# Kernel tuning notes

Hardware: AMD Instinct MI355X
Metric: run time of the kernel (lower is better)

Reference implementation:

```python
import jax, jax.numpy as jnp
import numpy as np
from functools import partial

# Straight-through sign (Binarize): sign forward, identity gradient
@jax.custom_vjp
def ste_sign(x):
    return jnp.sign(x)

def _ste_fwd(x):
    return jnp.sign(x), None

def _ste_bwd(_, g):
    return (g,)

ste_sign.defvjp(_ste_fwd, _ste_bwd)


def conv2d(x, w):
    # x: [N,C,H,W], w: [O,I,kh,kw], VALID conv, stride 1
    return jax.lax.conv_general_dilated(
        x, w, window_strides=(1, 1), padding='VALID',
        dimension_numbers=('NCHW', 'OIHW', 'NCHW'))


def maxpool2x2(x):
    return jax.lax.reduce_window(
        x, -jnp.inf, jax.lax.max, (1, 1, 2, 2), (1, 1, 2, 2), 'VALID')


def setup_inputs() -> dict:
    key = jax.random.key(0)
    ks = jax.random.split(key, 32)
    d = {}
    d['x'] = jax.random.normal(ks[0], (128, 3, 32, 32), dtype=jnp.float32)
    wshapes = [(128, 3, 3, 3), (128, 128, 3, 3), (256, 128, 3, 3),
               (256, 256, 3, 3), (512, 256, 3, 3), (512, 512, 3, 3),
               (10, 512, 4, 4)]
    for i, s in enumerate(wshapes):
        d[f'w{i+1}'] = jax.random.normal(ks[1 + i], s, dtype=jnp.float32) * 0.05
    bn_ch = [128, 128, 256, 256, 512, 512, 10]
    for i, c in enumerate(bn_ch):
        d[f'bn{i+1}_s'] = jax.random.uniform(ks[10 + 2 * i], (c,), dtype=jnp.float32,
                                             minval=0.5, maxval=1.5)
        d[f'bn{i+1}_t'] = jax.random.normal(ks[11 + 2 * i], (c,), dtype=jnp.float32) * 0.1
    return d


def _forward(x, w1, w2, w3, w4, w5, w6, w7,
             bn1_s, bn1_t, bn2_s, bn2_t, bn3_s, bn3_t, bn4_s, bn4_t,
             bn5_s, bn5_t, bn6_s, bn6_t, bn7_s, bn7_t):
    def block(h, w, s, t, pool, binarize_in):
        if binarize_in:
            h = ste_sign(h)            # binarize activations (in_ch != 3)
        h = jnp.pad(h, ((0, 0), (0, 0), (1, 1), (1, 1)))  # F.pad value=0
        h = conv2d(h, ste_sign(w))      # binarized weights
        if pool:
            h = maxpool2x2(h)
        h = h * s[None, :, None, None] + t[None, :, None, None]  # eval BN
        return jnp.clip(h, -1.0, 1.0)   # Hardtanh

    h = block(x, w1, bn1_s, bn1_t, pool=False, binarize_in=False)  # 32x32x128
    h = block(h, w2, bn2_s, bn2_t, pool=True,  binarize_in=True)   # 16x16x128
    h = block(h, w3, bn3_s, bn3_t, pool=False, binarize_in=True)   # 16x16x256
    h = block(h, w4, bn4_s, bn4_t, pool=True,  binarize_in=True)   # 8x8x256
    h = block(h, w5, bn5_s, bn5_t, pool=False, binarize_in=True)   # 8x8x512
    h = block(h, w6, bn6_s, bn6_t, pool=True,  binarize_in=True)   # 4x4x512
    # conv7: binarize input + weights, 4x4 kernel, no padding -> [N,10,1,1]
    h = conv2d(ste_sign(h), ste_sign(w7))
    h = h.reshape(-1, 10)
    h = h * bn7_s + bn7_t               # eval BatchNorm1d(10)
    return jax.nn.log_softmax(h, axis=1)


def reference(x, w1, w2, w3, w4, w5, w6, w7,
              bn1_s, bn1_t, bn2_s, bn2_t, bn3_s, bn3_t, bn4_s, bn4_t,
              bn5_s, bn5_t, bn6_s, bn6_t, bn7_s, bn7_t):
    return _forward(x, w1, w2, w3, w4, w5, w6, w7,
                    bn1_s, bn1_t, bn2_s, bn2_t, bn3_s, bn3_t, bn4_s, bn4_t,
                    bn5_s, bn5_t, bn6_s, bn6_t, bn7_s, bn7_t)
```

## Files before the change

kernel.cpp:

```cpp
#include <hip/hip_runtime.h>
#include <cstdint>
#include <math.h>

#define NB 128

__global__ void pack_all_kernel(
    const float* __restrict__ w2, const float* __restrict__ w3,
    const float* __restrict__ w4, const float* __restrict__ w5,
    const float* __restrict__ w6, const float* __restrict__ w7,
    uint32_t* __restrict__ wp2, uint32_t* __restrict__ wp3,
    uint32_t* __restrict__ wp4, uint32_t* __restrict__ wp5,
    uint32_t* __restrict__ wp6, uint32_t* __restrict__ wp7) {
  int i = blockIdx.x * 256 + threadIdx.x;
  const float* w; uint32_t* wp; int C, KHW; bool nl = true;
  if (i < 4608)        { w = w2; wp = wp2; C = 128; KHW = 9; }
  else if (i < 13824)  { i -= 4608;   w = w3; wp = wp3; C = 128; KHW = 9; }
  else if (i < 32256)  { i -= 13824;  w = w4; wp = wp4; C = 256; KHW = 9; }
  else if (i < 69120)  { i -= 32256;  w = w5; wp = wp5; C = 256; KHW = 9; }
  else if (i < 142848) { i -= 69120;  w = w6; wp = wp6; C = 512; KHW = 9; }
  else if (i < 145408) { i -= 142848; w = w7; wp = wp7; C = 512; KHW = 16; nl = false; }
  else return;
  int Cw = C >> 5;
  int cw = i % Cw;
  int rest = i / Cw;
  int t = rest % KHW;
  int o = rest / KHW;
  uint32_t word = 0;
  for (int b = 0; b < 32; ++b)
    word |= ((w[(o * C + cw * 32 + b) * KHW + t] >= 0.0f) ? 1u : 0u) << b;
  if (nl) wp[(((o >> 6) * KHW + t) * Cw + cw) * 64 + (o & 63)] = word;
  else    wp[(o * KHW + t) * Cw + cw] = word;
}

__global__ __launch_bounds__(256) void conv1_kernel(
    const float* __restrict__ x, const float* __restrict__ w1,
    const float* __restrict__ bs, const float* __restrict__ bt,
    uint32_t* __restrict__ out) {
  const int ocw = blockIdx.y;
  __shared__ float wlds[27 * 32];
  __shared__ float sl[32], tl[32];
  for (int i = threadIdx.x; i < 27 * 32; i += 256) {
    int oc = i & 31, k = i >> 5;
    float v = w1[(ocw * 32 + oc) * 27 + k];
    wlds[k * 32 + oc] = (v >= 0.0f) ? 1.0f : -1.0f;
  }
  if (threadIdx.x < 32) {
    sl[threadIdx.x] = bs[ocw * 32 + threadIdx.x];
    tl[threadIdx.x] = bt[ocw * 32 + threadIdx.x];
  }
  __syncthreads();
  int p = blockIdx.x * 256 + threadIdx.x;
  int px = p & 31, py = (p >> 5) & 31, n = p >> 10;
  double acc[32];
#pragma unroll
  for (int oc = 0; oc < 32; ++oc) acc[oc] = 0.0;
  for (int ic = 0; ic < 3; ++ic) {
    for (int kh = 0; kh < 3; ++kh) {
      int yy = py + kh - 1;
      if ((unsigned)yy >= 32u) continue;
      for (int kw = 0; kw < 3; ++kw) {
        int xx = px + kw - 1;
        if ((unsigned)xx >= 32u) continue;
        double xv = (double)x[((n * 3 + ic) * 32 + yy) * 32 + xx];
        int k = ic * 9 + kh * 3 + kw;
#pragma unroll
        for (int oc = 0; oc < 32; ++oc)
          acc[oc] += (wlds[k * 32 + oc] >= 0.0f) ? xv : -xv;
      }
    }
  }
  uint32_t word = 0;
#pragma unroll
  for (int oc = 0; oc < 32; ++oc) {
    double v = acc[oc] * (double)sl[oc] + (double)tl[oc];
    word |= (v >= 0.0 ? 1u : 0u) << oc;
  }
  out[p * 4 + ocw] = word;
}

template <int CW, int H, int W, int PC, int R, bool POOL, int MINW>
__global__ __launch_bounds__(64, MINW) void bconv_kernel(
    const uint32_t* __restrict__ act, const uint32_t* __restrict__ wpk,
    const float* __restrict__ bs, const float* __restrict__ bt,
    uint32_t* __restrict__ out, int OCW) {
  const int lane = threadIdx.x;
  const int ocg = blockIdx.y;
  const int cpr = W / PC;
  const int c = blockIdx.x;
  const int cg = c % cpr;
  const int rg = (c / cpr) % (H / R);
  const int n  = c / (cpr * (H / R));
  const int y0 = rg * R, x0 = cg * PC;

  uint32_t wreg[9 * CW];
#pragma unroll
  for (int t = 0; t < 9; ++t)
#pragma unroll
    for (int cw = 0; cw < CW; ++cw)
      wreg[t * CW + cw] = wpk[(((ocg * 9) + t) * CW + cw) * 64 + lane];

  int acc[R * PC];
#pragma unroll
  for (int p = 0; p < R * PC; ++p) acc[p] = 0;

#pragma unroll
  for (int ry = -1; ry <= R; ++ry) {
    const int y = y0 + ry;
    if (y < 0 || y >= H) continue;
#pragma unroll
    for (int cc = -1; cc <= PC; ++cc) {
      const int x = x0 + cc;
      if (x < 0 || x >= W) continue;
      const uint32_t* ap = act + ((n * H + y) * W + x) * CW;
      uint32_t av[CW];
#pragma unroll
      for (int cw = 0; cw < CW; ++cw) av[cw] = ap[cw];
#pragma unroll
      for (int r = 0; r < R; ++r) {
        const int kh = ry - r + 1;
        if (kh < 0 || kh > 2) continue;
#pragma unroll
        for (int kw = 0; kw < 3; ++kw) {
          const int pxo = cc - kw + 1;
          if (pxo < 0 || pxo >= PC) continue;
#pragma unroll
          for (int cw = 0; cw < CW; ++cw)
            acc[r * PC + pxo] += __popc(av[cw] ^ wreg[(kh * 3 + kw) * CW + cw]);
        }
      }
    }
  }

  const double sd = (double)bs[ocg * 64 + lane];
  const double td = (double)bt[ocg * 64 + lane];
  if (!POOL) {
    uint64_t bal[R * PC];
#pragma unroll
    for (int r = 0; r < R; ++r)
#pragma unroll
      for (int pxo = 0; pxo < PC; ++pxo) {
        const int y = y0 + r, x = x0 + pxo;
        const int nv = CW * (3 - (y == 0) - (y == H - 1)) * (3 - (x == 0) - (x == W - 1));
        double v = (double)(32 * nv - 2 * acc[r * PC + pxo]) * sd + td;
        bal[r * PC + pxo] = __ballot(v >= 0.0);
      }
    if (lane == 0) {
#pragma unroll
      for (int r = 0; r < R; ++r)
#pragma unroll
        for (int pxo = 0; pxo < PC; ++pxo) {
          uint32_t* o = out + ((n * H + (y0 + r)) * W + (x0 + pxo)) * OCW + ocg * 2;
          uint64_t m = bal[r * PC + pxo];
          o[0] = (uint32_t)m; o[1] = (uint32_t)(m >> 32);
        }
    }
  } else {
    static_assert(!POOL || R == 2, "pool needs row pairs");
    uint64_t pooled[PC / 2];
#pragma unroll
    for (int c2 = 0; c2 < PC / 2; ++c2) pooled[c2] = 0;
#pragma unroll
    for (int r = 0; r < R; ++r)
#pragma unroll
      for (int pxo = 0; pxo < PC; ++pxo) {
        const int y = y0 + r, x = x0 + pxo;
        const int nv = CW * (3 - (y == 0) - (y == H - 1)) * (3 - (x == 0) - (x == W - 1));
        double v = (double)(32 * nv - 2 * acc[r * PC + pxo]) * sd + td;
        pooled[pxo >> 1] |= __ballot(v >= 0.0);
      }
    if (lane == 0) {
#pragma unroll
      for (int c2 = 0; c2 < PC / 2; ++c2) {
        const int yo = y0 >> 1, xo = (x0 >> 1) + c2;
        uint32_t* o = out + ((n * (H / 2) + yo) * (W / 2) + xo) * OCW + ocg * 2;
        o[0] = (uint32_t)pooled[c2]; o[1] = (uint32_t)(pooled[c2] >> 32);
      }
    }
  }
}

__global__ __launch_bounds__(64) void conv7_kernel(
    const uint32_t* __restrict__ act, const uint32_t* __restrict__ wp,
    const float* __restrict__ bs, const float* __restrict__ bt,
    float* __restrict__ out) {
  int n = blockIdx.x;
  int lane = threadIdx.x;
  const uint32_t* a = act + n * 256;
  __shared__ double logits[10];
  for (int o = 0; o < 10; ++o) {
    int acc = 0;
    for (int w = lane; w < 256; w += 64) acc += __popc(a[w] ^ wp[o * 256 + w]);
    for (int off = 32; off > 0; off >>= 1) acc += __shfl_down(acc, off, 64);
    if (lane == 0) {
      double dotd = (double)(8192 - 2 * acc);
      logits[o] = dotd * (double)bs[o] + (double)bt[o];
    }
  }
  __syncthreads();
  if (lane == 0) {
    double m = logits[0];
    for (int o = 1; o < 10; ++o) m = fmax(m, logits[o]);
    double s = 0.0;
    for (int o = 0; o < 10; ++o) s += exp(logits[o] - m);
    double lse = log(s);
    for (int o = 0; o < 10; ++o) out[n * 10 + o] = (float)(logits[o] - m - lse);
  }
}

extern "C" void kernel_launch(void* const* d_in, const int* in_sizes, int n_in,
                              void* d_out, int out_size, void* d_ws, size_t ws_size,
                              hipStream_t stream) {
  const float* x  = (const float*)d_in[0];
  const float* w1 = (const float*)d_in[1];
  const float* w2 = (const float*)d_in[2];
  const float* w3 = (const float*)d_in[3];
  const float* w4 = (const float*)d_in[4];
  const float* w5 = (const float*)d_in[5];
  const float* w6 = (const float*)d_in[6];
  const float* w7 = (const float*)d_in[7];
  const float* s1 = (const float*)d_in[8];  const float* t1 = (const float*)d_in[9];
  const float* s2 = (const float*)d_in[10]; const float* t2 = (const float*)d_in[11];
  const float* s3 = (const float*)d_in[12]; const float* t3 = (const float*)d_in[13];
  const float* s4 = (const float*)d_in[14]; const float* t4 = (const float*)d_in[15];
  const float* s5 = (const float*)d_in[16]; const float* t5 = (const float*)d_in[17];
  const float* s6 = (const float*)d_in[18]; const float* t6 = (const float*)d_in[19];
  const float* s7 = (const float*)d_in[20]; const float* t7 = (const float*)d_in[21];
  float* out = (float*)d_out;

  uint32_t* ws = (uint32_t*)d_ws;
  uint32_t* A   = ws;
  uint32_t* B   = ws + 524288;
  uint32_t* wp2 = ws + 1048576;
  uint32_t* wp3 = wp2 + 4608;
  uint32_t* wp4 = wp3 + 9216;
  uint32_t* wp5 = wp4 + 18432;
  uint32_t* wp6 = wp5 + 36864;
  uint32_t* wp7 = wp6 + 73728;

  pack_all_kernel<<<dim3(568), dim3(256), 0, stream>>>(
      w2, w3, w4, w5, w6, w7, wp2, wp3, wp4, wp5, wp6, wp7);

  conv1_kernel<<<dim3(512, 4), dim3(256), 0, stream>>>(x, w1, s1, t1, A);

  bconv_kernel<4, 32, 32, 8, 2, true, 4>
      <<<dim3(8192, 2), dim3(64), 0, stream>>>(A, wp2, s2, t2, B, 4);

  bconv_kernel<4, 16, 16, 16, 1, false, 4>
      <<<dim3(2048, 4), dim3(64), 0, stream>>>(B, wp3, s3, t3, A, 8);

  bconv_kernel<8, 16, 16, 8, 2, true, 4>
      <<<dim3(2048, 4), dim3(64), 0, stream>>>(A, wp4, s4, t4, B, 8);

  bconv_kernel<8, 8, 8, 8, 2, false, 4>
      <<<dim3(512, 8), dim3(64), 0, stream>>>(B, wp5, s5, t5, A, 16);

  bconv_kernel<16, 8, 8, 8, 2, true, 2>
      <<<dim3(512, 8), dim3(64), 0, stream>>>(A, wp6, s6, t6, B, 16);

  conv7_kernel<<<dim3(128), dim3(64), 0, stream>>>(B, wp7, s7, t7, out);
}
```

Measured before the change: 328.8 us.

## Bit-pack conv1 weights, tile conv1 per wave, split bconv channel passes

Conv1 becomes a 64-lane kernel where each lane owns one output channel and handles a tile of 2x8 pixels. It reads the sign-packed weights as 64-bit lane masks, filled by an extra step in the packing kernel, instead of staging ±1 floats in shared memory for 32 channels per thread. The binarized conv kernel gains a CWP parameter that loads weights in channel-word chunks, so the largest layer can hold fewer weight registers and run at higher occupancy. Launch-bound wave counts are raised for several layers, which risks register spills.

```diff
diff --git a/kernel.cpp b/kernel.cpp
--- a/kernel.cpp
+++ b/kernel.cpp
@@ -5,21 +5,32 @@
 #define NB 128
 
 __global__ void pack_all_kernel(
+    const float* __restrict__ w1,
     const float* __restrict__ w2, const float* __restrict__ w3,
     const float* __restrict__ w4, const float* __restrict__ w5,
     const float* __restrict__ w6, const float* __restrict__ w7,
+    uint32_t* __restrict__ wp1,
     uint32_t* __restrict__ wp2, uint32_t* __restrict__ wp3,
     uint32_t* __restrict__ wp4, uint32_t* __restrict__ wp5,
     uint32_t* __restrict__ wp6, uint32_t* __restrict__ wp7) {
   int i = blockIdx.x * 256 + threadIdx.x;
+  if (i >= 145516) return;
+  if (i >= 145408) {
+    int j = i - 145408;
+    int ocg = j / 54, rem = j % 54, t = rem >> 1, half = rem & 1;
+    uint32_t word = 0;
+    for (int b = 0; b < 32; ++b)
+      word |= ((w1[(ocg * 64 + half * 32 + b) * 27 + t] >= 0.0f) ? 1u : 0u) << b;
+    wp1[(ocg * 27 + t) * 2 + half] = word;
+    return;
+  }
   const float* w; uint32_t* wp; int C, KHW; bool nl = true;
   if (i < 4608)        { w = w2; wp = wp2; C = 128; KHW = 9; }
   else if (i < 13824)  { i -= 4608;   w = w3; wp = wp3; C = 128; KHW = 9; }
   else if (i < 32256)  { i -= 13824;  w = w4; wp = wp4; C = 256; KHW = 9; }
   else if (i < 69120)  { i -= 32256;  w = w5; wp = wp5; C = 256; KHW = 9; }
   else if (i < 142848) { i -= 69120;  w = w6; wp = wp6; C = 512; KHW = 9; }
-  else if (i < 145408) { i -= 142848; w = w7; wp = wp7; C = 512; KHW = 16; nl = false; }
-  else return;
+  else                 { i -= 142848; w = w7; wp = wp7; C = 512; KHW = 16; nl = false; }
   int Cw = C >> 5;
   int cw = i % Cw;
   int rest = i / Cw;
@@ -32,57 +43,92 @@
   else    wp[(o * KHW + t) * Cw + cw] = word;
 }
 
-__global__ __launch_bounds__(256) void conv1_kernel(
-    const float* __restrict__ x, const float* __restrict__ w1,
+__device__ __forceinline__ bool lane_bit(uint64_t m, int lane) {
+#if __has_builtin(__builtin_amdgcn_inverse_ballot_w64)
+  (void)lane;
+  return __builtin_amdgcn_inverse_ballot_w64(m);
+#else
+  return (m >> lane) & 1;
+#endif
+}
+
+template <int PC, int R>
+__global__ __launch_bounds__(64, 6) void conv1_kernel(
+    const float* __restrict__ x, const uint32_t* __restrict__ wp1,
     const float* __restrict__ bs, const float* __restrict__ bt,
     uint32_t* __restrict__ out) {
-  const int ocw = blockIdx.y;
-  __shared__ float wlds[27 * 32];
-  __shared__ float sl[32], tl[32];
-  for (int i = threadIdx.x; i < 27 * 32; i += 256) {
-    int oc = i & 31, k = i >> 5;
-    float v = w1[(ocw * 32 + oc) * 27 + k];
-    wlds[k * 32 + oc] = (v >= 0.0f) ? 1.0f : -1.0f;
-  }
-  if (threadIdx.x < 32) {
-    sl[threadIdx.x] = bs[ocw * 32 + threadIdx.x];
-    tl[threadIdx.x] = bt[ocw * 32 + threadIdx.x];
-  }
-  __syncthreads();
-  int p = blockIdx.x * 256 + threadIdx.x;
-  int px = p & 31, py = (p >> 5) & 31, n = p >> 10;
-  double acc[32];
-#pragma unroll
-  for (int oc = 0; oc < 32; ++oc) acc[oc] = 0.0;
+  const int lane = threadIdx.x;
+  const int ocg = blockIdx.y;
+  const int cpr = 32 / PC;
+  const int c = blockIdx.x;
+  const int cg = c % cpr;
+  const int rg = (c / cpr) % (32 / R);
+  const int n  = c / (cpr * (32 / R));
+  const int y0 = rg * R, x0 = cg * PC;
+
+  double acc[R * PC];
+#pragma unroll
+  for (int p = 0; p < R * PC; ++p) acc[p] = 0.0;
+
+  const uint64_t* wm64 = (const uint64_t*)wp1;
   for (int ic = 0; ic < 3; ++ic) {
-    for (int kh = 0; kh < 3; ++kh) {
-      int yy = py + kh - 1;
-      if ((unsigned)yy >= 32u) continue;
-      for (int kw = 0; kw < 3; ++kw) {
-        int xx = px + kw - 1;
-        if ((unsigned)xx >= 32u) continue;
-        double xv = (double)x[((n * 3 + ic) * 32 + yy) * 32 + xx];
-        int k = ic * 9 + kh * 3 + kw;
-#pragma unroll
-        for (int oc = 0; oc < 32; ++oc)
-          acc[oc] += (wlds[k * 32 + oc] >= 0.0f) ? xv : -xv;
-      }
-    }
-  }
-  uint32_t word = 0;
-#pragma unroll
-  for (int oc = 0; oc < 32; ++oc) {
-    double v = acc[oc] * (double)sl[oc] + (double)tl[oc];
-    word |= (v >= 0.0 ? 1u : 0u) << oc;
-  }
-  out[p * 4 + ocw] = word;
-}
-
-template <int CW, int H, int W, int PC, int R, bool POOL, int MINW>
+    uint64_t wm[9];
+#pragma unroll
+    for (int t = 0; t < 9; ++t) wm[t] = wm64[ocg * 27 + ic * 9 + t];
+#pragma unroll
+    for (int ey = -1; ey <= R; ++ey) {
+      const int y = y0 + ey;
+      if (y < 0 || y >= 32) continue;
+#pragma unroll
+      for (int ex = -1; ex <= PC; ++ex) {
+        const int xx = x0 + ex;
+        if (xx < 0 || xx >= 32) continue;
+        const double xd = (double)x[((n * 3 + ic) * 32 + y) * 32 + xx];
+#pragma unroll
+        for (int r = 0; r < R; ++r) {
+          const int kh = ey - r + 1;
+          if (kh < 0 || kh > 2) continue;
+#pragma unroll
+          for (int kw = 0; kw < 3; ++kw) {
+            const int pxo = ex - kw + 1;
+            if (pxo < 0 || pxo >= PC) continue;
+            const bool neg = lane_bit(wm[kh * 3 + kw], lane) == false;
+            acc[r * PC + pxo] += neg ? -xd : xd;
+          }
+        }
+      }
+    }
+  }
+
+  const double sd = (double)bs[ocg * 64 + lane];
+  const double td = (double)bt[ocg * 64 + lane];
+  uint64_t bal[R * PC];
+#pragma unroll
+  for (int r = 0; r < R; ++r)
+#pragma unroll
+    for (int pxo = 0; pxo < PC; ++pxo) {
+      double v = acc[r * PC + pxo] * sd + td;
+      bal[r * PC + pxo] = __ballot(v >= 0.0);
+    }
+  if (lane == 0) {
+#pragma unroll
+    for (int r = 0; r < R; ++r)
+#pragma unroll
+      for (int pxo = 0; pxo < PC; ++pxo) {
+        const int p = ((n * 32 + (y0 + r)) * 32 + (x0 + pxo));
+        uint32_t* o = out + p * 4 + ocg * 2;
+        uint64_t m = bal[r * PC + pxo];
+        o[0] = (uint32_t)m; o[1] = (uint32_t)(m >> 32);
+      }
+  }
+}
+
+template <int CW, int CWP, int H, int W, int PC, int R, bool POOL, int MINW>
 __global__ __launch_bounds__(64, MINW) void bconv_kernel(
     const uint32_t* __restrict__ act, const uint32_t* __restrict__ wpk,
     const float* __restrict__ bs, const float* __restrict__ bt,
     uint32_t* __restrict__ out, int OCW) {
+  static_assert(CW % CWP == 0, "");
   const int lane = threadIdx.x;
   const int ocg = blockIdx.y;
   const int cpr = W / PC;
@@ -92,40 +138,43 @@
   const int n  = c / (cpr * (H / R));
   const int y0 = rg * R, x0 = cg * PC;
 
-  uint32_t wreg[9 * CW];
-#pragma unroll
-  for (int t = 0; t < 9; ++t)
-#pragma unroll
-    for (int cw = 0; cw < CW; ++cw)
-      wreg[t * CW + cw] = wpk[(((ocg * 9) + t) * CW + cw) * 64 + lane];
-
   int acc[R * PC];
 #pragma unroll
   for (int p = 0; p < R * PC; ++p) acc[p] = 0;
 
 #pragma unroll
-  for (int ry = -1; ry <= R; ++ry) {
-    const int y = y0 + ry;
-    if (y < 0 || y >= H) continue;
-#pragma unroll
-    for (int cc = -1; cc <= PC; ++cc) {
-      const int x = x0 + cc;
-      if (x < 0 || x >= W) continue;
-      const uint32_t* ap = act + ((n * H + y) * W + x) * CW;
-      uint32_t av[CW];
-#pragma unroll
-      for (int cw = 0; cw < CW; ++cw) av[cw] = ap[cw];
-#pragma unroll
-      for (int r = 0; r < R; ++r) {
-        const int kh = ry - r + 1;
-        if (kh < 0 || kh > 2) continue;
-#pragma unroll
-        for (int kw = 0; kw < 3; ++kw) {
-          const int pxo = cc - kw + 1;
-          if (pxo < 0 || pxo >= PC) continue;
-#pragma unroll
-          for (int cw = 0; cw < CW; ++cw)
-            acc[r * PC + pxo] += __popc(av[cw] ^ wreg[(kh * 3 + kw) * CW + cw]);
+  for (int pass = 0; pass < CW / CWP; ++pass) {
+    uint32_t wreg[9 * CWP];
+#pragma unroll
+    for (int t = 0; t < 9; ++t)
+#pragma unroll
+      for (int cw = 0; cw < CWP; ++cw)
+        wreg[t * CWP + cw] = wpk[(((ocg * 9) + t) * CW + pass * CWP + cw) * 64 + lane];
+
+#pragma unroll
+    for (int ry = -1; ry <= R; ++ry) {
+      const int y = y0 + ry;
+      if (y < 0 || y >= H) continue;
+#pragma unroll
+      for (int cc = -1; cc <= PC; ++cc) {
+        const int x = x0 + cc;
+        if (x < 0 || x >= W) continue;
+        const uint32_t* ap = act + ((n * H + y) * W + x) * CW + pass * CWP;
+        uint32_t av[CWP];
+#pragma unroll
+        for (int cw = 0; cw < CWP; ++cw) av[cw] = ap[cw];
+#pragma unroll
+        for (int r = 0; r < R; ++r) {
+          const int kh = ry - r + 1;
+          if (kh < 0 || kh > 2) continue;
+#pragma unroll
+          for (int kw = 0; kw < 3; ++kw) {
+            const int pxo = cc - kw + 1;
+            if (pxo < 0 || pxo >= PC) continue;
+#pragma unroll
+            for (int cw = 0; cw < CWP; ++cw)
+              acc[r * PC + pxo] += __popc(av[cw] ^ wreg[(kh * 3 + kw) * CWP + cw]);
+          }
         }
       }
     }
@@ -236,25 +285,26 @@
   uint32_t* wp5 = wp4 + 18432;
   uint32_t* wp6 = wp5 + 36864;
   uint32_t* wp7 = wp6 + 73728;
-
-  pack_all_kernel<<<dim3(568), dim3(256), 0, stream>>>(
-      w2, w3, w4, w5, w6, w7, wp2, wp3, wp4, wp5, wp6, wp7);
-
-  conv1_kernel<<<dim3(512, 4), dim3(256), 0, stream>>>(x, w1, s1, t1, A);
-
-  bconv_kernel<4, 32, 32, 8, 2, true, 4>
+  uint32_t* wp1 = wp7 + 2560;
+
+  pack_all_kernel<<<dim3(569), dim3(256), 0, stream>>>(
+      w1, w2, w3, w4, w5, w6, w7, wp1, wp2, wp3, wp4, wp5, wp6, wp7);
+
+  conv1_kernel<8, 2><<<dim3(8192, 2), dim3(64), 0, stream>>>(x, wp1, s1, t1, A);
+
+  bconv_kernel<4, 4, 32, 32, 8, 2, true, 6>
       <<<dim3(8192, 2), dim3(64), 0, stream>>>(A, wp2, s2, t2, B, 4);
 
-  bconv_kernel<4, 16, 16, 16, 1, false, 4>
+  bconv_kernel<4, 4, 16, 16, 16, 1, false, 6>
       <<<dim3(2048, 4), dim3(64), 0, stream>>>(B, wp3, s3, t3, A, 8);
 
-  bconv_kernel<8, 16, 16, 8, 2, true, 4>
+  bconv_kernel<8, 8, 16, 16, 8, 2, true, 4>
       <<<dim3(2048, 4), dim3(64), 0, stream>>>(A, wp4, s4, t4, B, 8);
 
-  bconv_kernel<8, 8, 8, 8, 2, false, 4>
+  bconv_kernel<8, 8, 8, 8, 8, 2, false, 4>
       <<<dim3(512, 8), dim3(64), 0, stream>>>(B, wp5, s5, t5, A, 16);
 
-  bconv_kernel<16, 8, 8, 8, 2, true, 2>
+  bconv_kernel<16, 8, 8, 8, 8, 2, true, 4>
       <<<dim3(512, 8), dim3(64), 0, stream>>>(A, wp6, s6, t6, B, 16);
 
   conv7_kernel<<<dim3(128), dim3(64), 0, stream>>>(B, wp7, s7, t7, out);
```

Measured after the change: 322.4 us. No clear change (-1.9%).
